# Performance work log

Hardware: AMD Instinct MI355X
Metric: run time of the kernel (lower is better)

The kernel has to match this reference:

```python
import jax, jax.numpy as jnp
import numpy as np

B, L, H, GRID = 16, 4096, 1152, 64  # L = GRID*GRID patches


def setup_inputs() -> dict:
    key = jax.random.key(0)
    k1, = jax.random.split(key, 1)
    hidden_states = jax.random.normal(k1, (B, L, H), dtype=jnp.float32)
    # row-major 64x64 grid of (x, y) patch positions, same for every batch element
    idx = jnp.arange(L)
    pos = jnp.stack([idx % GRID, idx // GRID], axis=-1)  # [L, 2]
    pixel_position_ids = jnp.broadcast_to(pos, (B, L, 2)).astype(jnp.int64)
    padding_positions = jnp.zeros((B, L), dtype=bool)
    return {
        "hidden_states": hidden_states,
        "pixel_position_ids": pixel_position_ids,
        "padding_positions": padding_positions,
        "output_length": 1024,
    }


def reference(hidden_states, pixel_position_ids, padding_positions, output_length):
    hidden_size = hidden_states.shape[-1]
    root_hidden_size = hidden_size ** 0.5
    in_len = hidden_states.shape[1]

    # zero out padded patches
    hs = jnp.where(padding_positions[..., None], 0.0, hidden_states)

    if in_len != output_length:
        k = int((in_len // output_length) ** 0.5)
        k_sq = k * k
        assert k_sq * output_length == in_len
        clamped = jnp.maximum(pixel_position_ids, 0)                      # [B, L, 2]
        max_x = jnp.max(clamped[..., 0], axis=-1, keepdims=True) + 1      # [B, 1]
        kidx = clamped // k
        seg = kidx[..., 0] + (max_x // k) * kidx[..., 1]                  # [B, L] segment ids in [0, output_length)

        # segment mean == (one_hot/k^2)^T @ hs, but without the dense one-hot
        def pool_one(seg_b, hs_b):
            summed = jax.ops.segment_sum(hs_b.astype(jnp.float32), seg_b,
                                          num_segments=output_length)     # [out_len, H]
            counts = jax.ops.segment_sum(jnp.ones((in_len,), jnp.float32), seg_b,
                                          num_segments=output_length)     # [out_len]
            return summed / k_sq, counts > 0

        pooled, mask = jax.vmap(pool_one)(seg, hs)
        hs = pooled.astype(hidden_states.dtype)
        padding_positions = mask

    hs = hs * root_hidden_size
    return hs, padding_positions
```

## Files before the change

kernel.cpp:

```cpp
#include <hip/hip_runtime.h>

#define BB 16
#define LL 4096
#define HH 1152
#define OUT_LEN 1024
#define KK 2
#define CAP 8
#define H4 (HH / 4)
#define H8 (HH / 8)

typedef float vf4 __attribute__((ext_vector_type(4)));

__global__ void maxx_zero_kernel(const int* __restrict__ pos, int* __restrict__ maxx,
                                 int* __restrict__ cnt) {
    const int b = blockIdx.x;
    const int tid = threadIdx.x;
    #pragma unroll
    for (int j = 0; j < OUT_LEN / 256; ++j) cnt[b * OUT_LEN + j * 256 + tid] = 0;

    int m = 0;
    for (int i = tid; i < LL; i += 256) {
        int x = pos[((size_t)b * LL + i) * 2];
        m = max(m, max(x, 0));
    }
    __shared__ int sm[256];
    sm[tid] = m;
    __syncthreads();
    for (int s = 128; s > 0; s >>= 1) {
        if (tid < s) sm[tid] = max(sm[tid], sm[tid + s]);
        __syncthreads();
    }
    if (tid == 0) maxx[b] = sm[0] + 1;
}

__global__ void build_inv(const int* __restrict__ pos, const int* __restrict__ pad,
                          const int* __restrict__ maxx,
                          int* __restrict__ cnt, int* __restrict__ inv) {
    const int fl = blockIdx.x * 256 + threadIdx.x;
    const int b = fl >> 12;
    const int i = fl & (LL - 1);
    int x = max(pos[2 * (size_t)fl], 0);
    int y = max(pos[2 * (size_t)fl + 1], 0);
    const int segw = maxx[b] / KK;
    const int seg = x / KK + segw * (y / KK);
    const int base = b * OUT_LEN + seg;
    const int slot = atomicAdd(&cnt[base], 1);
    if (slot < CAP) inv[base * CAP + slot] = pad[fl] ? (i | 0x80000000) : i;
}

__global__ __launch_bounds__(256) void gather_pool(
    const float* __restrict__ hs, const int* __restrict__ cnt, const int* __restrict__ inv,
    float* __restrict__ out) {
    const int id = blockIdx.x * 256 + threadIdx.x;
    const int h8 = id % H8;
    const int t  = id / H8;
    const int b  = t >> 10;

    const int c  = cnt[t];
    const int cc = min(c, CAP);

    const vf4* __restrict__ hp = (const vf4*)hs;
    vf4 a0 = (vf4)0.0f;
    vf4 a1 = (vf4)0.0f;
    #pragma unroll 4
    for (int j = 0; j < cc; ++j) {
        const int ii = inv[t * CAP + j];
        if (ii >= 0) {
            const vf4* p = hp + (size_t)(b * LL + ii) * H4 + h8 * 2;
            a0 += __builtin_nontemporal_load(p);
            a1 += __builtin_nontemporal_load(p + 1);
        }
    }
    const float scale = 8.485281374238571f;
    a0 *= scale;
    a1 *= scale;

    vf4* op = (vf4*)out + (size_t)t * H4 + h8 * 2;
    __builtin_nontemporal_store(a0, op);
    __builtin_nontemporal_store(a1, op + 1);

    if (h8 == 0) out[(size_t)BB * OUT_LEN * HH + t] = (c > 0) ? 1.0f : 0.0f;
}

extern "C" void kernel_launch(void* const* d_in, const int* in_sizes, int n_in,
                              void* d_out, int out_size, void* d_ws, size_t ws_size,
                              hipStream_t stream) {
    const float* hs  = (const float*)d_in[0];
    const int*   pos = (const int*)d_in[1];
    const int*   pad = (const int*)d_in[2];
    float* out = (float*)d_out;

    int* ws   = (int*)d_ws;
    int* maxx = ws;
    int* cnt  = ws + 64;
    int* inv  = cnt + BB * OUT_LEN;

    maxx_zero_kernel<<<BB, 256, 0, stream>>>(pos, maxx, cnt);
    build_inv<<<(BB * LL) / 256, 256, 0, stream>>>(pos, pad, maxx, cnt, inv);
    gather_pool<<<(BB * OUT_LEN * H8) / 256, 256, 0, stream>>>(hs, cnt, inv, out);
}
```

Before: 418.8 us.

## Add fast path for canonical row-major grid with fixed 2x2 gather

The prep kernel now checks, per batch, whether positions form the canonical 64-wide row-major grid with no padding, and sets a flag. When the flag is set, build_inv exits early and gather_pool reads the four 2x2 neighbours directly by computed address, with no atomics and no inverse-index lookups. The per-thread column mapping also changes from two adjacent float4 values to two values split half a row apart, which alters coalescing. The general path is kept for inputs that are not canonical, so correctness holds, but a runtime validation pass is added.

```diff
diff --git a/kernel.cpp b/kernel.cpp
--- a/kernel.cpp
+++ b/kernel.cpp
@@ -8,36 +8,49 @@
 #define CAP 8
 #define H4 (HH / 4)
 #define H8 (HH / 8)
+#define GRID_W 64
 
 typedef float vf4 __attribute__((ext_vector_type(4)));
 
-__global__ void maxx_zero_kernel(const int* __restrict__ pos, int* __restrict__ maxx,
-                                 int* __restrict__ cnt) {
+__global__ __launch_bounds__(1024) void prep_kernel(const int* __restrict__ pos,
+                                                    const int* __restrict__ pad,
+                                                    int* __restrict__ maxx,
+                                                    int* __restrict__ flag,
+                                                    int* __restrict__ cnt) {
     const int b = blockIdx.x;
     const int tid = threadIdx.x;
-    #pragma unroll
-    for (int j = 0; j < OUT_LEN / 256; ++j) cnt[b * OUT_LEN + j * 256 + tid] = 0;
+    cnt[b * OUT_LEN + tid] = 0;
 
     int m = 0;
-    for (int i = tid; i < LL; i += 256) {
-        int x = pos[((size_t)b * LL + i) * 2];
-        m = max(m, max(x, 0));
+    int canon = 1;
+    const int2* __restrict__ pp = (const int2*)pos;
+    #pragma unroll
+    for (int j = 0; j < LL / 1024; ++j) {
+        const int i = j * 1024 + tid;
+        const int2 q = pp[(size_t)b * LL + i];
+        m = max(m, max(q.x, 0));
+        canon &= (q.x == (i & (GRID_W - 1))) & (q.y == (i >> 6)) & (pad[b * LL + i] == 0);
     }
-    __shared__ int sm[256];
-    sm[tid] = m;
+    __shared__ int sm[1024];
+    __shared__ int sc[1024];
+    sm[tid] = m; sc[tid] = canon;
     __syncthreads();
-    for (int s = 128; s > 0; s >>= 1) {
-        if (tid < s) sm[tid] = max(sm[tid], sm[tid + s]);
+    for (int s = 512; s > 0; s >>= 1) {
+        if (tid < s) { sm[tid] = max(sm[tid], sm[tid + s]); sc[tid] &= sc[tid + s]; }
         __syncthreads();
     }
-    if (tid == 0) maxx[b] = sm[0] + 1;
+    if (tid == 0) {
+        maxx[b] = sm[0] + 1;
+        flag[b] = sc[0] & ((sm[0] + 1) == GRID_W);
+    }
 }
 
 __global__ void build_inv(const int* __restrict__ pos, const int* __restrict__ pad,
-                          const int* __restrict__ maxx,
+                          const int* __restrict__ maxx, const int* __restrict__ flag,
                           int* __restrict__ cnt, int* __restrict__ inv) {
     const int fl = blockIdx.x * 256 + threadIdx.x;
     const int b = fl >> 12;
+    if (flag[b]) return;
     const int i = fl & (LL - 1);
     int x = max(pos[2 * (size_t)fl], 0);
     int y = max(pos[2 * (size_t)fl + 1], 0);
@@ -50,36 +63,57 @@
 
 __global__ __launch_bounds__(256) void gather_pool(
     const float* __restrict__ hs, const int* __restrict__ cnt, const int* __restrict__ inv,
-    float* __restrict__ out) {
+    const int* __restrict__ flag, float* __restrict__ out) {
     const int id = blockIdx.x * 256 + threadIdx.x;
     const int h8 = id % H8;
     const int t  = id / H8;
     const int b  = t >> 10;
 
-    const int c  = cnt[t];
-    const int cc = min(c, CAP);
-
     const vf4* __restrict__ hp = (const vf4*)hs;
     vf4 a0 = (vf4)0.0f;
     vf4 a1 = (vf4)0.0f;
-    #pragma unroll 4
-    for (int j = 0; j < cc; ++j) {
-        const int ii = inv[t * CAP + j];
-        if (ii >= 0) {
-            const vf4* p = hp + (size_t)(b * LL + ii) * H4 + h8 * 2;
-            a0 += __builtin_nontemporal_load(p);
-            a1 += __builtin_nontemporal_load(p + 1);
+    float maskv = 1.0f;
+
+    if (flag[b]) {
+        const int s  = t & (OUT_LEN - 1);
+        const int sx = s & 31;
+        const int sy = s >> 5;
+        const int i0 = (sx << 1) + (sy << 7);
+        const vf4* p = hp + (size_t)(b * LL + i0) * H4 + h8;
+        vf4 r0 = __builtin_nontemporal_load(p);
+        vf4 r1 = __builtin_nontemporal_load(p + H4);
+        vf4 r2 = __builtin_nontemporal_load(p + 64 * H4);
+        vf4 r3 = __builtin_nontemporal_load(p + 65 * H4);
+        vf4 r4 = __builtin_nontemporal_load(p + H8);
+        vf4 r5 = __builtin_nontemporal_load(p + H4 + H8);
+        vf4 r6 = __builtin_nontemporal_load(p + 64 * H4 + H8);
+        vf4 r7 = __builtin_nontemporal_load(p + 65 * H4 + H8);
+        a0 = (r0 + r1) + (r2 + r3);
+        a1 = (r4 + r5) + (r6 + r7);
+    } else {
+        const int c  = cnt[t];
+        const int cc = min(c, CAP);
+        #pragma unroll 4
+        for (int j = 0; j < cc; ++j) {
+            const int ii = inv[t * CAP + j];
+            if (ii >= 0) {
+                const vf4* p = hp + (size_t)(b * LL + ii) * H4 + h8;
+                a0 += __builtin_nontemporal_load(p);
+                a1 += __builtin_nontemporal_load(p + H8);
+            }
         }
+        maskv = (c > 0) ? 1.0f : 0.0f;
     }
+
     const float scale = 8.485281374238571f;
     a0 *= scale;
     a1 *= scale;
 
-    vf4* op = (vf4*)out + (size_t)t * H4 + h8 * 2;
+    vf4* op = (vf4*)out + (size_t)t * H4 + h8;
     __builtin_nontemporal_store(a0, op);
-    __builtin_nontemporal_store(a1, op + 1);
+    __builtin_nontemporal_store(a1, op + H8);
 
-    if (h8 == 0) out[(size_t)BB * OUT_LEN * HH + t] = (c > 0) ? 1.0f : 0.0f;
+    if (h8 == 0) out[(size_t)BB * OUT_LEN * HH + t] = maskv;
 }
 
 extern "C" void kernel_launch(void* const* d_in, const int* in_sizes, int n_in,
@@ -92,10 +126,11 @@
 
     int* ws   = (int*)d_ws;
     int* maxx = ws;
-    int* cnt  = ws + 64;
+    int* flag = ws + 64;
+    int* cnt  = ws + 128;
     int* inv  = cnt + BB * OUT_LEN;
 
-    maxx_zero_kernel<<<BB, 256, 0, stream>>>(pos, maxx, cnt);
-    build_inv<<<(BB * LL) / 256, 256, 0, stream>>>(pos, pad, maxx, cnt, inv);
-    gather_pool<<<(BB * OUT_LEN * H8) / 256, 256, 0, stream>>>(hs, cnt, inv, out);
+    prep_kernel<<<BB, 1024, 0, stream>>>(pos, pad, maxx, flag, cnt);
+    build_inv<<<(BB * LL) / 256, 256, 0, stream>>>(pos, pad, maxx, flag, cnt, inv);
+    gather_pool<<<(BB * OUT_LEN * H8) / 256, 256, 0, stream>>>(hs, cnt, inv, flag, out);
 }
```

Result: faster. 403.1 us (-3.7%).
